# Kernel tuning notes

Hardware: AMD Instinct MI355X
Metric: run time of the kernel (lower is better)

## Reference

```python
import jax, jax.numpy as jnp
import numpy as np

N = 50000      # nodes
E = 400000     # lower-adjacency edges (avg degree 8)
D = 128        # input_dim == output_dim (o_dim in DEC_HOGNN)
GEO = 20       # geo_dim
H = 3          # heads
C = 128        # out_channels per head
NUM_LAYERS = 3


def _lin_init(key, fan_in, fan_out, extra=()):
    s = 1.0 / np.sqrt(fan_in)
    return jax.random.uniform(key, extra + (fan_in, fan_out), jnp.float32, -s, s)


def setup_inputs() -> dict:
    key = jax.random.key(0)
    ks = jax.random.split(key, 20)
    inp = {
        "h": jax.random.normal(ks[0], (N, D), jnp.float32),
        "lower_adj_feat": jax.random.normal(ks[1], (E, GEO), jnp.float32),
        "dir_w": jax.random.normal(ks[2], (E, 1), jnp.float32),
        "src_idx": jax.random.randint(ks[3], (E,), 0, N),
        "dst_idx": jax.random.randint(ks[4], (E,), 0, N),
        # edge_encoder: Linear(2*D + geo + 1 -> D)
        "W_ee": _lin_init(ks[5], 2 * D + GEO + 1, D),
        "b_ee": jnp.zeros((D,), jnp.float32),
        # residual linear (layer 0 only; others Identity)
        "W_res": _lin_init(ks[6], D, D),
        "b_res": jnp.zeros((D,), jnp.float32),
        # 3 TransformerConv layers, all in=D out=C heads=H (stacked)
        "Wq": _lin_init(ks[7], D, H * C, (NUM_LAYERS,)),
        "bq": jnp.zeros((NUM_LAYERS, H * C), jnp.float32),
        "Wk": _lin_init(ks[8], D, H * C, (NUM_LAYERS,)),
        "bk": jnp.zeros((NUM_LAYERS, H * C), jnp.float32),
        "Wv": _lin_init(ks[9], D, H * C, (NUM_LAYERS,)),
        "bv": jnp.zeros((NUM_LAYERS, H * C), jnp.float32),
        "We": _lin_init(ks[10], D, H * C, (NUM_LAYERS,)),
        "be": jnp.zeros((NUM_LAYERS, H * C), jnp.float32),
        # lin_skip: in -> out_channels (concat=False)
        "Ws": _lin_init(ks[11], D, C, (NUM_LAYERS,)),
        "bs": jnp.zeros((NUM_LAYERS, C), jnp.float32),
        # ctr_lin: Linear(input_dim + output_dim -> output_dim)
        "W_ctr": _lin_init(ks[12], 2 * D, D),
        "b_ctr": jnp.zeros((D,), jnp.float32),
    }
    return inp


def _transformer_conv(x, src, dst, e_attr, Wq, bq, Wk, bk, Wv, bv, We, be, Ws, bs):
    """PyG TransformerConv, heads=H, concat=False (head mean), root skip."""
    n = x.shape[0]
    q = (x @ Wq + bq).reshape(n, H, C)
    k = (x @ Wk + bk).reshape(n, H, C)
    v = (x @ Wv + bv).reshape(n, H, C)
    e = (e_attr @ We + be).reshape(-1, H, C)      # [E,H,C]
    ke = k[src] + e                                # edge-conditioned keys
    alpha = (q[dst] * ke).sum(-1) / jnp.sqrt(jnp.asarray(C, x.dtype))  # [E,H]
    # segment softmax over destination nodes
    amax = jax.ops.segment_max(alpha, dst, num_segments=n)
    amax = jnp.where(jnp.isfinite(amax), amax, 0.0)
    ex = jnp.exp(alpha - amax[dst])
    den = jax.ops.segment_sum(ex, dst, num_segments=n)
    w = ex / (den[dst] + 1e-16)
    msg = (v[src] + e) * w[:, :, None]             # [E,H,C]
    out = jax.ops.segment_sum(msg.reshape(-1, H * C), dst, num_segments=n)
    out = out.reshape(n, H, C).mean(axis=1)        # concat=False -> head mean
    return out + x @ Ws + bs                       # root weight skip


def reference(h, lower_adj_feat, dir_w, src_idx, dst_idx,
              W_ee, b_ee, W_res, b_res,
              Wq, bq, Wk, bk, Wv, bv, We, be, Ws, bs,
              W_ctr, b_ctr):
    # edge encoder: [h[dst], h[src]*dir, dir, geo] -> D
    edge_features = jnp.concatenate(
        [h[dst_idx], h[src_idx] * dir_w, dir_w, lower_adj_feat], axis=-1)
    edge_attr = edge_features @ W_ee + b_ee
    h_cur = h
    for i in range(NUM_LAYERS):
        residual = (h_cur @ W_res + b_res) if i == 0 else h_cur
        h_t = _transformer_conv(h_cur, src_idx, dst_idx, edge_attr,
                                Wq[i], bq[i], Wk[i], bk[i], Wv[i], bv[i],
                                We[i], be[i], Ws[i], bs[i])
        h_cur = jax.nn.relu(h_t + residual)
    return jnp.concatenate([h, h_cur], axis=-1) @ W_ctr + b_ctr
```

## Files before the change

### kernel.cpp

```cpp
#include <hip/hip_runtime.h>
#include <math.h>

#define NN 50000
#define NE 400000

typedef _Float16 f16;
typedef _Float16 f16x8 __attribute__((ext_vector_type(8)));
typedef _Float16 f16x4 __attribute__((ext_vector_type(4)));
typedef _Float16 f16x2 __attribute__((ext_vector_type(2)));
typedef float f32x4 __attribute__((ext_vector_type(4)));

static __device__ __forceinline__ float dot8(f16x8 a, f16x8 b, float acc) {
#if defined(__has_builtin) && __has_builtin(__builtin_amdgcn_fdot2)
#pragma unroll
  for (int j = 0; j < 4; ++j) {
    f16x2 x = {a[2 * j], a[2 * j + 1]};
    f16x2 y = {b[2 * j], b[2 * j + 1]};
    acc = __builtin_amdgcn_fdot2(x, y, acc, false);
  }
#else
#pragma unroll
  for (int j = 0; j < 8; ++j) acc += (float)a[j] * (float)b[j];
#endif
  return acc;
}

#if defined(__has_builtin) && __has_builtin(__builtin_amdgcn_global_load_lds)
#define HAVE_GLL 1
static __device__ __forceinline__ void gload_lds16(const f16* gp, f16* lp) {
  __builtin_amdgcn_global_load_lds((const __attribute__((address_space(1))) void*)gp,
                                   (__attribute__((address_space(3))) void*)lp, 16, 0, 0);
}
#else
#define HAVE_GLL 0
#endif

__global__ __launch_bounds__(256) void hgemm_k128_kernel(
    const f16* __restrict__ A, int lda,
    const f16* __restrict__ WT,
    const float* __restrict__ bias,
    f16* __restrict__ outb, int ldb,
    int M, int ntiles)
{
  __shared__ f16 As[128 * 128];
  __shared__ f16 Bs[64 * 128];
  const int t = threadIdx.x;
  const int wv = t >> 6, lane = t & 63;
  const int l15 = lane & 15, l4 = lane >> 4;
  const int c8 = lane & 15, rsub = lane >> 4;
  const int row0 = blockIdx.x * 128;

#if HAVE_GLL
#pragma unroll
  for (int k = 0; k < 8; ++k) {
    int r = wv * 4 + k * 16 + rsub;
    int rc = row0 + r; if (rc >= M) rc = M - 1;
    const f16* gp = A + (size_t)rc * lda + ((c8 ^ (r & 15)) << 3);
    gload_lds16(gp, As + (wv * 4 + k * 16) * 128);
  }
#else
  for (int i = t; i < 2048; i += 256) {
    int r = i >> 4, cc = i & 15;
    int gr = row0 + r; if (gr >= M) gr = M - 1;
    float4 v = *(const float4*)(A + (size_t)gr * lda + cc * 8);
    *(float4*)(As + r * 128 + ((cc ^ (r & 15)) << 3)) = v;
  }
#endif
  for (int ct = 0; ct < ntiles; ++ct) {
    const int col0 = (blockIdx.y * ntiles + ct) * 64;
#if HAVE_GLL
#pragma unroll
    for (int k = 0; k < 4; ++k) {
      int c = wv * 4 + k * 16 + rsub;
      const f16* gp = WT + (size_t)(col0 + c) * 128 + ((c8 ^ (c & 15)) << 3);
      gload_lds16(gp, Bs + (wv * 4 + k * 16) * 128);
    }
#else
    for (int i = t; i < 1024; i += 256) {
      int c = i >> 4, cc = i & 15;
      float4 v = *(const float4*)(WT + (size_t)(col0 + c) * 128 + cc * 8);
      *(float4*)(Bs + c * 128 + ((cc ^ (c & 15)) << 3)) = v;
    }
#endif
    __syncthreads();
    f32x4 acc[2][4];
#pragma unroll
    for (int m = 0; m < 2; ++m)
#pragma unroll
      for (int n = 0; n < 4; ++n) acc[m][n] = (f32x4){0.f, 0.f, 0.f, 0.f};
#pragma unroll
    for (int ks = 0; ks < 4; ++ks) {
      const int co = (((ks * 4 + l4) ^ l15) << 3);
      f16x8 a0 = *(const f16x8*)(As + (wv * 32 +      l15) * 128 + co);
      f16x8 a1 = *(const f16x8*)(As + (wv * 32 + 16 + l15) * 128 + co);
      f16x8 b0 = *(const f16x8*)(Bs + (     l15) * 128 + co);
      f16x8 b1 = *(const f16x8*)(Bs + (16 + l15) * 128 + co);
      f16x8 b2 = *(const f16x8*)(Bs + (32 + l15) * 128 + co);
      f16x8 b3 = *(const f16x8*)(Bs + (48 + l15) * 128 + co);
      acc[0][0] = __builtin_amdgcn_mfma_f32_16x16x32_f16(a0, b0, acc[0][0], 0, 0, 0);
      acc[0][1] = __builtin_amdgcn_mfma_f32_16x16x32_f16(a0, b1, acc[0][1], 0, 0, 0);
      acc[0][2] = __builtin_amdgcn_mfma_f32_16x16x32_f16(a0, b2, acc[0][2], 0, 0, 0);
      acc[0][3] = __builtin_amdgcn_mfma_f32_16x16x32_f16(a0, b3, acc[0][3], 0, 0, 0);
      acc[1][0] = __builtin_amdgcn_mfma_f32_16x16x32_f16(a1, b0, acc[1][0], 0, 0, 0);
      acc[1][1] = __builtin_amdgcn_mfma_f32_16x16x32_f16(a1, b1, acc[1][1], 0, 0, 0);
      acc[1][2] = __builtin_amdgcn_mfma_f32_16x16x32_f16(a1, b2, acc[1][2], 0, 0, 0);
      acc[1][3] = __builtin_amdgcn_mfma_f32_16x16x32_f16(a1, b3, acc[1][3], 0, 0, 0);
    }
    __syncthreads();
    float bv4[4];
#pragma unroll
    for (int n = 0; n < 4; ++n) bv4[n] = bias ? bias[col0 + n * 16 + l15] : 0.f;
#pragma unroll
    for (int m = 0; m < 2; ++m) {
#pragma unroll
      for (int j = 0; j < 4; ++j) {
        int r = row0 + wv * 32 + m * 16 + l4 * 4 + j;
        if (r >= M) continue;
#pragma unroll
        for (int n = 0; n < 4; ++n) {
          int c = col0 + n * 16 + l15;
          outb[(size_t)r * ldb + c] = (f16)(acc[m][n][j] + bv4[n]);
        }
      }
    }
  }
}

__global__ __launch_bounds__(256) void hgemm2_kernel(
    const f16* __restrict__ A, int lda,
    const f16* __restrict__ A2, int lda2, int a2k,
    const f16* __restrict__ WT, int K,
    const float* __restrict__ bias,
    float* __restrict__ outf,
    f16* __restrict__ outb, int ldb,
    const f16* __restrict__ fresid, int ldr,
    int dorelu, int M)
{
  __shared__ f16 As[128 * 128];
  __shared__ f16 Bs[128 * 128];
  const int t = threadIdx.x;
  const int wv = t >> 6, lane = t & 63;
  const int l15 = lane & 15, l4 = lane >> 4;
  const int c8 = lane & 15, rsub = lane >> 4;
  const int row0 = blockIdx.x * 128;
  const int col0 = blockIdx.y * 128;

  f32x4 acc[2][8];
#pragma unroll
  for (int m = 0; m < 2; ++m)
#pragma unroll
    for (int n = 0; n < 8; ++n) acc[m][n] = (f32x4){0.f, 0.f, 0.f, 0.f};

  for (int kc = 0; kc < K; kc += 128) {
    const f16* Ap; int koff, ldA;
    if (kc >= a2k) { Ap = A2; koff = kc - a2k; ldA = lda2; }
    else           { Ap = A;  koff = kc;       ldA = lda;  }
#if HAVE_GLL
#pragma unroll
    for (int k = 0; k < 8; ++k) {
      int r = wv * 4 + k * 16 + rsub;
      int rc = row0 + r; if (rc >= M) rc = M - 1;
      const f16* gp = Ap + (size_t)rc * ldA + koff + ((c8 ^ (r & 15)) << 3);
      gload_lds16(gp, As + (wv * 4 + k * 16) * 128);
    }
#pragma unroll
    for (int k = 0; k < 8; ++k) {
      int c = wv * 4 + k * 16 + rsub;
      const f16* gp = WT + (size_t)(col0 + c) * K + kc + ((c8 ^ (c & 15)) << 3);
      gload_lds16(gp, Bs + (wv * 4 + k * 16) * 128);
    }
#else
    for (int i = t; i < 2048; i += 256) {
      int r = i >> 4, cc = i & 15;
      int gr = row0 + r; if (gr >= M) gr = M - 1;
      float4 v = *(const float4*)(Ap + (size_t)gr * ldA + koff + cc * 8);
      *(float4*)(As + r * 128 + ((cc ^ (r & 15)) << 3)) = v;
    }
    for (int i = t; i < 2048; i += 256) {
      int c = i >> 4, cc = i & 15;
      float4 v = *(const float4*)(WT + (size_t)(col0 + c) * K + kc + cc * 8);
      *(float4*)(Bs + c * 128 + ((cc ^ (c & 15)) << 3)) = v;
    }
#endif
    __syncthreads();
#pragma unroll
    for (int ks = 0; ks < 4; ++ks) {
      const int co = (((ks * 4 + l4) ^ l15) << 3);
      f16x8 a0 = *(const f16x8*)(As + (wv * 32 +      l15) * 128 + co);
      f16x8 a1 = *(const f16x8*)(As + (wv * 32 + 16 + l15) * 128 + co);
#pragma unroll
      for (int n = 0; n < 8; ++n) {
        f16x8 b = *(const f16x8*)(Bs + (n * 16 + l15) * 128 + co);
        acc[0][n] = __builtin_amdgcn_mfma_f32_16x16x32_f16(a0, b, acc[0][n], 0, 0, 0);
        acc[1][n] = __builtin_amdgcn_mfma_f32_16x16x32_f16(a1, b, acc[1][n], 0, 0, 0);
      }
    }
    __syncthreads();
  }

  float bv8[8];
#pragma unroll
  for (int n = 0; n < 8; ++n) bv8[n] = bias ? bias[col0 + n * 16 + l15] : 0.f;
#pragma unroll
  for (int m = 0; m < 2; ++m) {
#pragma unroll
    for (int j = 0; j < 4; ++j) {
      int r = row0 + wv * 32 + m * 16 + l4 * 4 + j;
      if (r >= M) continue;
#pragma unroll
      for (int n = 0; n < 8; ++n) {
        int c = col0 + n * 16 + l15;
        float val = acc[m][n][j] + bv8[n];
        if (fresid) val += (float)fresid[(size_t)r * ldr + c];
        if (dorelu) val = fmaxf(val, 0.f);
        if (outb) outb[(size_t)r * ldb + c] = (f16)val;
        else      outf[(size_t)r * 128 + c] = val;
      }
    }
  }
}

__global__ void zero_int_kernel(int* __restrict__ p, int n) {
  int i = blockIdx.x * 256 + threadIdx.x;
  if (i < n) p[i] = 0;
}
__global__ void hist_kernel(const int* __restrict__ dst, int* __restrict__ deg) {
  int e = blockIdx.x * 256 + threadIdx.x;
  if (e < NE) atomicAdd(&deg[dst[e]], 1);
}
__global__ void scanA_kernel(const int* __restrict__ deg, int* __restrict__ rowstart,
                             int* __restrict__ part) {
  __shared__ int sd[256];
  int b = blockIdx.x, t = threadIdx.x, i = b * 256 + t;
  sd[t] = (i < NN) ? deg[i] : 0;
  __syncthreads();
  for (int o = 1; o < 256; o <<= 1) {
    int v = (t >= o) ? sd[t - o] : 0;
    __syncthreads();
    sd[t] += v;
    __syncthreads();
  }
  if (i < NN) rowstart[i + 1] = sd[t];
  if (t == 255) part[b] = sd[255];
}
__global__ void scanB_kernel(int* __restrict__ part, int nb) {
  __shared__ int sd[256];
  int t = threadIdx.x;
  sd[t] = (t < nb) ? part[t] : 0;
  __syncthreads();
  for (int o = 1; o < 256; o <<= 1) {
    int v = (t >= o) ? sd[t - o] : 0;
    __syncthreads();
    sd[t] += v;
    __syncthreads();
  }
  if (t < nb) part[t] = sd[t];
}
__global__ void scanC_kernel(const int* __restrict__ deg, int* __restrict__ rowstart,
                             const int* __restrict__ part, int* __restrict__ cursor) {
  int b = blockIdx.x, t = threadIdx.x, i = b * 256 + t;
  if (i >= NN) return;
  int off = b ? part[b - 1] : 0;
  int fin = rowstart[i + 1] + off;
  rowstart[i + 1] = fin;
  cursor[i] = fin - deg[i];
  if (i == 0) rowstart[0] = 0;
}
__global__ void scatter_kernel(const int* __restrict__ dst, const int* __restrict__ src,
                               const float* __restrict__ dirw, const float* __restrict__ geo,
                               int* __restrict__ cursor,
                               int* __restrict__ srcp, f16* __restrict__ dirpb,
                               f16* __restrict__ geop) {
  int e = blockIdx.x * 256 + threadIdx.x;
  if (e < NE) {
    int pos = atomicAdd(&cursor[dst[e]], 1);
    srcp[pos] = src[e];
    float dv = dirw[e];
    dirpb[pos] = (f16)dv;
    f16* gp = geop + (size_t)pos * 24;
#pragma unroll
    for (int j = 0; j < 20; ++j) gp[j] = (f16)geo[(size_t)e * 20 + j];
    gp[20] = (f16)dv;
    gp[21] = (f16)0.f; gp[22] = (f16)0.f; gp[23] = (f16)0.f;
  }
}

__global__ void prep_kernel(const float* __restrict__ Wee, const float* __restrict__ bee,
                            const float* __restrict__ WeAll, const float* __restrict__ beAll,
                            float* __restrict__ matsAll)
{
  const int layer = blockIdx.y;
  const float* We = WeAll + (size_t)layer * 49152;
  const float* be = beAll + (size_t)layer * 384;
  float* mats = matsAll + (size_t)layer * 132352;
  int idx = blockIdx.x * 256 + threadIdx.x;
  if (idx >= 132352) return;
  float acc = 0.0f;
  if (idx < 49152) {
    int h = idx >> 14, rem = idx & 16383, c = rem >> 7, u = rem & 127;
    for (int j = 0; j < 128; ++j)
      acc += We[(size_t)j * 384 + h * 128 + c] * Wee[(size_t)(128 + u) * 128 + j];
    mats[idx] = acc;
  } else if (idx < 58368) {
    int r = idx - 49152; int h = r / 3072; int rem = r - h * 3072; int c = rem / 24; int u = rem - c * 24;
    if (u < 21) {
      int trow = (u < 20) ? (257 + u) : 256;
      for (int j = 0; j < 128; ++j)
        acc += We[(size_t)j * 384 + h * 128 + c] * Wee[(size_t)trow * 128 + j];
    }
    mats[idx] = acc;
  } else if (idx < 107520) {
    int r = idx - 58368; int h = r >> 14; int rem = r & 16383; int tt = rem >> 7; int c = rem & 127;
    for (int j = 0; j < 128; ++j)
      acc += Wee[(size_t)(128 + tt) * 128 + j] * We[(size_t)j * 384 + h * 128 + c];
    mats[idx] = acc;
  } else if (idx < 115584) {
    int r = idx - 107520; int h = r / 2688; int rem = r - h * 2688; int tt = rem >> 7; int c = rem & 127;
    int trow = (tt < 20) ? (257 + tt) : 256;
    for (int j = 0; j < 128; ++j)
      acc += Wee[(size_t)trow * 128 + j] * We[(size_t)j * 384 + h * 128 + c];
    mats[idx] = acc;
  } else if (idx < 115968) {
    int r = idx - 115584; int h = r >> 7; int c = r & 127;
    for (int j = 0; j < 128; ++j)
      acc += bee[j] * We[(size_t)j * 384 + h * 128 + c];
    mats[idx] = acc + be[h * 128 + c];
  } else {
    int r = idx - 115968; int tt = r >> 7; int c = r & 127;
    for (int j = 0; j < 128; ++j)
      acc += Wee[(size_t)tt * 128 + j] *
             (We[(size_t)j * 384 + c] + We[(size_t)j * 384 + 128 + c] + We[(size_t)j * 384 + 256 + c]);
    mats[idx] = acc * (1.0f / 3.0f);
  }
}

__global__ void prepB_kernel(const float* __restrict__ Wq, const float* __restrict__ bq,
                             const float* __restrict__ Wk, const float* __restrict__ matsAll,
                             f16* __restrict__ WABT, float* __restrict__ biasAB)
{
  int idx = blockIdx.x * 256 + threadIdx.x;
  if (idx < 344064) {
    int i = idx / 114688; int r = idx % 114688; int c = r >> 7; int k = r & 127;
    float acc = 0.f;
    if (c < 384) {
      int h = c >> 7, u = c & 127;
      const float* wq = Wq + ((size_t)i * 128 + k) * 384 + h * 128;
      const float* wk = Wk + ((size_t)i * 128 + u) * 384 + h * 128;
      for (int c2 = 0; c2 < 128; ++c2) acc += wq[c2] * wk[c2];
    } else if (c < 768) {
      int h = (c - 384) >> 7, u = (c - 384) & 127;
      const float* wq = Wq + ((size_t)i * 128 + k) * 384 + h * 128;
      const float* m2 = matsAll + (size_t)i * 132352 + h * 16384 + u;
      for (int c2 = 0; c2 < 128; ++c2) acc += wq[c2] * m2[c2 * 128];
    } else if (c < 840) {
      int h = (c - 768) / 24, tt = (c - 768) % 24;
      const float* wq = Wq + ((size_t)i * 128 + k) * 384 + h * 128;
      const float* m34 = matsAll + (size_t)i * 132352 + 49152 + h * 3072 + tt;
      for (int c2 = 0; c2 < 128; ++c2) acc += wq[c2] * m34[c2 * 24];
    }
    WABT[(size_t)i * 114688 + c * 128 + k] = (f16)acc;
  } else if (idx < 346752) {
    int r = idx - 344064; int i = r / 896; int c = r % 896;
    float acc = 0.f;
    if (c < 384) {
      int h = c >> 7, u = c & 127;
      const float* bqv = bq + i * 384 + h * 128;
      const float* wk = Wk + ((size_t)i * 128 + u) * 384 + h * 128;
      for (int c2 = 0; c2 < 128; ++c2) acc += bqv[c2] * wk[c2];
    } else if (c < 768) {
      int h = (c - 384) >> 7, u = (c - 384) & 127;
      const float* bqv = bq + i * 384 + h * 128;
      const float* m2 = matsAll + (size_t)i * 132352 + h * 16384 + u;
      for (int c2 = 0; c2 < 128; ++c2) acc += bqv[c2] * m2[c2 * 128];
    } else if (c < 840) {
      int h = (c - 768) / 24, tt = (c - 768) % 24;
      const float* bqv = bq + i * 384 + h * 128;
      const float* m34 = matsAll + (size_t)i * 132352 + 49152 + h * 3072 + tt;
      for (int c2 = 0; c2 < 128; ++c2) acc += bqv[c2] * m34[c2 * 24];
    }
    biasAB[i * 896 + c] = acc;
  }
}

__global__ void prep2_kernel(const float* __restrict__ matsAll, const float* __restrict__ Wv,
                             const float* __restrict__ bv, const float* __restrict__ Ws,
                             const float* __restrict__ Wres, f16* __restrict__ W2bigT)
{
  int idx = blockIdx.x * 256 + threadIdx.x;
  if (idx >= 442368) return;
  int i = idx / 147456; int r = idx % 147456; int c = r / 1152; int k = r % 1152;
  float v = 0.f;
  if (k < 384) {
    int h = k >> 7, tt = k & 127;
    v = matsAll[(size_t)i * 132352 + 58368 + h * 16384 + tt * 128 + c];
  } else if (k < 768) {
    int h = (k - 384) >> 7, u = (k - 384) & 127;
    v = Wv[((size_t)i * 128 + u) * 384 + h * 128 + c];
  } else if (k < 840) {
    int h = (k - 768) / 24, tt = (k - 768) % 24;
    if (tt < 21)       v = matsAll[(size_t)i * 132352 + 107520 + h * 2688 + tt * 128 + c];
    else if (tt == 21) v = matsAll[(size_t)i * 132352 + 115584 + h * 128 + c]
                         + bv[i * 384 + h * 128 + c];
  } else if (k < 896) {
    v = 0.f;
  } else if (k < 1024) {
    v = matsAll[(size_t)i * 132352 + 115968 + (k - 896) * 128 + c];
  } else {
    v = Ws[((size_t)i * 128 + (k - 1024)) * 128 + c];
    if (i == 0) v += Wres[(k - 1024) * 128 + c];
  }
  W2bigT[(size_t)i * 147456 + c * 1152 + k] = (f16)v;
}

__global__ void wprep_kernel(const float* __restrict__ Wctr, const float* __restrict__ bs,
                             const float* __restrict__ bres,
                             f16* __restrict__ WctrT2, float* __restrict__ bias0)
{
  int idx = blockIdx.x * 256 + threadIdx.x;
  if (idx < 32768) {
    int c = idx >> 8, k = idx & 255;
    float v = (k < 128) ? Wctr[(size_t)(128 + k) * 128 + c]
                        : Wctr[(size_t)(k - 128) * 128 + c];
    WctrT2[idx] = (f16)v;
  } else if (idx < 32896) {
    int c = idx - 32768;
    bias0[c] = bs[c] + bres[c];
  }
}

__global__ __launch_bounds__(256) void attn_kernel(
    const f16* __restrict__ xh,
    f16* __restrict__ nbuf,
    const int* __restrict__ rowstart,
    const int* __restrict__ srcp,
    const f16* __restrict__ dirpb,
    const f16* __restrict__ geop)
{
  const int sl = threadIdx.x & 15;
  const int n = blockIdx.x * 16 + (threadIdx.x >> 4);
  const float rsC = 0.088388347648318447f;
  f16* row = nbuf + (size_t)n * 1024;

  f16x8 qk[3], g2[3];
#pragma unroll
  for (int h = 0; h < 3; ++h) {
    qk[h] = *(const f16x8*)(row + h * 128 + sl * 8);
    g2[h] = *(const f16x8*)(row + 384 + h * 128 + sl * 8);
  }
  float g34a[3], g34c[3];
#pragma unroll
  for (int h = 0; h < 3; ++h) {
    g34a[h] = (float)row[768 + h * 24 + sl];
    g34c[h] = (sl < 8) ? (float)row[768 + h * 24 + 16 + sl] : 0.f;
  }
  float den[3] = {0.f, 0.f, 0.f};
  float F2[3][8], Fv[3][8];
#pragma unroll
  for (int h = 0; h < 3; ++h)
#pragma unroll
    for (int j = 0; j < 8; ++j) { F2[h][j] = 0.f; Fv[h][j] = 0.f; }
  float f34a[3] = {0.f, 0.f, 0.f}, f34c[3] = {0.f, 0.f, 0.f};

  const int beg = rowstart[n], end = rowstart[n + 1];
  int ii = beg;
  for (; ii + 1 < end; ii += 2) {
    const int s0 = srcp[ii], s1 = srcp[ii + 1];
    const float d0 = (float)dirpb[ii], d1 = (float)dirpb[ii + 1];
    const f16* p0 = xh + (size_t)s0 * 256 + sl * 8;
    const f16* p1 = xh + (size_t)s1 * 256 + sl * 8;
    f16x8 xv0 = *(const f16x8*)p0;
    f16x8 hv0 = *(const f16x8*)(p0 + 128);
    f16x8 xv1 = *(const f16x8*)p1;
    f16x8 hv1 = *(const f16x8*)(p1 + 128);
    const float gea0 = (float)geop[(size_t)ii * 24 + sl];
    const float geb0 = (sl < 8) ? (float)geop[(size_t)ii * 24 + 16 + sl] : 0.f;
    const float gea1 = (float)geop[(size_t)(ii + 1) * 24 + sl];
    const float geb1 = (sl < 8) ? (float)geop[(size_t)(ii + 1) * 24 + 16 + sl] : 0.f;

    float pa[6];
#pragma unroll
    for (int h = 0; h < 3; ++h) {
      pa[h]     = dot8(qk[h], xv0, 0.f) + d0 * dot8(g2[h], hv0, 0.f)
                + gea0 * g34a[h] + geb0 * g34c[h];
      pa[3 + h] = dot8(qk[h], xv1, 0.f) + d1 * dot8(g2[h], hv1, 0.f)
                + gea1 * g34a[h] + geb1 * g34c[h];
    }
#pragma unroll
    for (int off = 1; off < 16; off <<= 1) {
#pragma unroll
      for (int q = 0; q < 6; ++q) pa[q] += __shfl_xor(pa[q], off);
    }
    float w0[3], w1[3];
#pragma unroll
    for (int h = 0; h < 3; ++h) {
      w0[h] = __expf(pa[h] * rsC);
      w1[h] = __expf(pa[3 + h] * rsC);
      den[h] += w0[h] + w1[h];
    }
#pragma unroll
    for (int h = 0; h < 3; ++h) {
      const float wd0 = w0[h] * d0, wd1 = w1[h] * d1;
#pragma unroll
      for (int j = 0; j < 8; ++j) {
        F2[h][j] = fmaf(wd0, (float)hv0[j], fmaf(wd1, (float)hv1[j], F2[h][j]));
        Fv[h][j] = fmaf(w0[h], (float)xv0[j], fmaf(w1[h], (float)xv1[j], Fv[h][j]));
      }
      f34a[h] = fmaf(w0[h], gea0, fmaf(w1[h], gea1, f34a[h]));
      f34c[h] = fmaf(w0[h], geb0, fmaf(w1[h], geb1, f34c[h]));
    }
  }
  if (ii < end) {
    const int s0 = srcp[ii];
    const float d0 = (float)dirpb[ii];
    const f16* p0 = xh + (size_t)s0 * 256 + sl * 8;
    f16x8 xv0 = *(const f16x8*)p0;
    f16x8 hv0 = *(const f16x8*)(p0 + 128);
    const float gea0 = (float)geop[(size_t)ii * 24 + sl];
    const float geb0 = (sl < 8) ? (float)geop[(size_t)ii * 24 + 16 + sl] : 0.f;
    float pa[3];
#pragma unroll
    for (int h = 0; h < 3; ++h)
      pa[h] = dot8(qk[h], xv0, 0.f) + d0 * dot8(g2[h], hv0, 0.f)
            + gea0 * g34a[h] + geb0 * g34c[h];
#pragma unroll
    for (int off = 1; off < 16; off <<= 1) {
#pragma unroll
      for (int q = 0; q < 3; ++q) pa[q] += __shfl_xor(pa[q], off);
    }
#pragma unroll
    for (int h = 0; h < 3; ++h) {
      const float w = __expf(pa[h] * rsC);
      den[h] += w;
      const float wd = w * d0;
#pragma unroll
      for (int j = 0; j < 8; ++j) {
        F2[h][j] = fmaf(wd, (float)hv0[j], F2[h][j]);
        Fv[h][j] = fmaf(w, (float)xv0[j], Fv[h][j]);
      }
      f34a[h] = fmaf(w, gea0, f34a[h]);
      f34c[h] = fmaf(w, geb0, f34c[h]);
    }
  }

  float sc[3], swh[3];
#pragma unroll
  for (int h = 0; h < 3; ++h) {
    sc[h] = (1.f / 3.f) / (den[h] + 1e-16f);
    swh[h] = den[h] * sc[h];
  }
#pragma unroll
  for (int h = 0; h < 3; ++h) {
    f16x8 o1, o2;
#pragma unroll
    for (int j = 0; j < 8; ++j) {
      o1[j] = (f16)(F2[h][j] * sc[h]);
      o2[j] = (f16)(Fv[h][j] * sc[h]);
    }
    *(f16x8*)(row + h * 128 + sl * 8) = o1;
    *(f16x8*)(row + 384 + h * 128 + sl * 8) = o2;
  }
#pragma unroll
  for (int h = 0; h < 3; ++h) {
    row[768 + h * 24 + sl] = (f16)(f34a[h] * sc[h]);
    if (sl < 8) {
      float fcv = (sl == 5) ? swh[h] : f34c[h] * sc[h];
      row[768 + h * 24 + 16 + sl] = (f16)fcv;
    }
  }
  f16x8 ho = *(const f16x8*)(xh + (size_t)n * 256 + 128 + sl * 8);
  if (beg >= end) {
#pragma unroll
    for (int j = 0; j < 8; ++j) ho[j] = (f16)0.f;
  }
  *(f16x8*)(row + 896 + sl * 8) = ho;
}

__global__ void hconv_kernel(const float* __restrict__ src, f16* __restrict__ xh) {
  int i = blockIdx.x * 256 + threadIdx.x;
  if (i >= NN * 32) return;
  float4 a = ((const float4*)src)[i];
  f16x4 o;
  o[0] = (f16)a.x; o[1] = (f16)a.y; o[2] = (f16)a.z; o[3] = (f16)a.w;
  int r = i >> 5, c4 = i & 31;
  *(f16x4*)(xh + (size_t)r * 256 + c4 * 4) = o;
  *(f16x4*)(xh + (size_t)r * 256 + 128 + c4 * 4) = o;
}

extern "C" void kernel_launch(void* const* d_in, const int* in_sizes, int n_in,
                              void* d_out, int out_size, void* d_ws, size_t ws_size,
                              hipStream_t stream)
{
  (void)in_sizes; (void)n_in; (void)out_size; (void)ws_size;
  const float* h    = (const float*)d_in[0];
  const float* geo  = (const float*)d_in[1];
  const float* dirw = (const float*)d_in[2];
  const int*   src  = (const int*)d_in[3];
  const int*   dst  = (const int*)d_in[4];
  const float* Wee  = (const float*)d_in[5];
  const float* bee  = (const float*)d_in[6];
  const float* Wres = (const float*)d_in[7];
  const float* bres = (const float*)d_in[8];
  const float* Wq   = (const float*)d_in[9];
  const float* bq   = (const float*)d_in[10];
  const float* Wk   = (const float*)d_in[11];
  const float* bk   = (const float*)d_in[12];  (void)bk;
  const float* Wv   = (const float*)d_in[13];
  const float* bv   = (const float*)d_in[14];
  const float* We   = (const float*)d_in[15];
  const float* be   = (const float*)d_in[16];
  const float* Ws   = (const float*)d_in[17];
  const float* bs   = (const float*)d_in[18];
  const float* Wctr = (const float*)d_in[19];
  const float* bctr = (const float*)d_in[20];

  char* base = (char*)d_ws;
  size_t off = 0;
  auto take = [&](size_t bytes) -> char* {
    char* p = base + off;
    off += bytes;
    off = (off + 255) & ~(size_t)255;
    return p;
  };
  f16* nbuf     = (f16*)take((size_t)NN * 1024 * 2);
  f16* xh       = (f16*)take((size_t)NN * 256 * 2);
  float* mats   = (float*)take((size_t)3 * 132352 * 4);
  f16* WABT     = (f16*)take((size_t)3 * 114688 * 2);
  float* biasAB = (float*)take((size_t)3 * 896 * 4);
  f16* W2bigT   = (f16*)take((size_t)3 * 147456 * 2);
  f16* WctrT2   = (f16*)take(32768 * 2);
  float* bias0  = (float*)take(128 * 4);
  f16* dirpb    = (f16*)take((size_t)NE * 2);
  f16* geop     = (f16*)take((size_t)NE * 24 * 2);
  int* deg      = (int*)take((size_t)NN * 4);
  int* rowstart = (int*)take((size_t)(NN + 1) * 4);
  int* cursor   = (int*)take((size_t)NN * 4);
  int* srcp     = (int*)take((size_t)NE * 4);
  int* part     = (int*)take(256 * 4);

  zero_int_kernel<<<(NN + 255) / 256, 256, 0, stream>>>(deg, NN);
  hist_kernel<<<(NE + 255) / 256, 256, 0, stream>>>(dst, deg);
  scanA_kernel<<<196, 256, 0, stream>>>(deg, rowstart, part);
  scanB_kernel<<<1, 256, 0, stream>>>(part, 196);
  scanC_kernel<<<196, 256, 0, stream>>>(deg, rowstart, part, cursor);
  scatter_kernel<<<(NE + 255) / 256, 256, 0, stream>>>(dst, src, dirw, geo, cursor,
                                                       srcp, dirpb, geop);
  hconv_kernel<<<6250, 256, 0, stream>>>(h, xh);
  wprep_kernel<<<129, 256, 0, stream>>>(Wctr, bs, bres, WctrT2, bias0);
  prep_kernel<<<dim3(518, 3), 256, 0, stream>>>(Wee, bee, We, be, mats);
  prepB_kernel<<<(346752 + 255) / 256, 256, 0, stream>>>(Wq, bq, Wk, mats, WABT, biasAB);
  prep2_kernel<<<(442368 + 255) / 256, 256, 0, stream>>>(mats, Wv, bv, Ws, Wres, W2bigT);

  for (int i = 0; i < 3; ++i) {
    hgemm_k128_kernel<<<dim3(391, 2), 256, 0, stream>>>(xh, 256, WABT + (size_t)i * 114688,
        biasAB + (size_t)i * 896, nbuf, 1024, NN, 7);
    attn_kernel<<<3125, 256, 0, stream>>>(xh, nbuf, rowstart, srcp, dirpb, geop);
    const float* obias = (i == 0) ? bias0 : (bs + i * 128);
    const f16* resid = (i == 0) ? nullptr : xh;
    hgemm2_kernel<<<dim3(391, 1), 256, 0, stream>>>(nbuf, 1024, xh, 256, 1024,
        W2bigT + (size_t)i * 147456, 1152, obias, nullptr, xh, 256,
        resid, 256, 1, NN);
  }
  hgemm2_kernel<<<dim3(391, 1), 256, 0, stream>>>(xh, 256, nullptr, 256, 1 << 30,
      WctrT2, 256, bctr, (float*)d_out, nullptr, 0, nullptr, 0, 0, NN);
}
```

Before: 609.5 us.

## Fuse final ctr_lin GEMM into last layer's output GEMM epilogue

In the last layer, the output GEMM kernel now writes its relu'd fp16 tile into shared memory and immediately multiplies it by the ctr_lin weights. It then loads the original h half from xh and accumulates it, writing the final fp32 output directly. This removes a separate kernel launch and a re-read of the hidden state from global memory. In exchange it adds extra shared-memory traffic and synchronisation to that block, and clamps out-of-range rows when loading.

```diff
diff --git a/kernel.cpp b/kernel.cpp
--- a/kernel.cpp
+++ b/kernel.cpp
@@ -131,10 +131,11 @@
     const f16* __restrict__ A2, int lda2, int a2k,
     const f16* __restrict__ WT, int K,
     const float* __restrict__ bias,
-    float* __restrict__ outf,
     f16* __restrict__ outb, int ldb,
     const f16* __restrict__ fresid, int ldr,
-    int dorelu, int M)
+    int dorelu, int M,
+    const f16* __restrict__ ctrW, const float* __restrict__ ctrB,
+    float* __restrict__ ctrOut)
 {
   __shared__ f16 As[128 * 128];
   __shared__ f16 Bs[128 * 128];
@@ -205,16 +206,82 @@
   for (int m = 0; m < 2; ++m) {
 #pragma unroll
     for (int j = 0; j < 4; ++j) {
-      int r = row0 + wv * 32 + m * 16 + l4 * 4 + j;
-      if (r >= M) continue;
+      int rl = wv * 32 + m * 16 + l4 * 4 + j;
+      int r = row0 + rl;
 #pragma unroll
       for (int n = 0; n < 8; ++n) {
         int c = col0 + n * 16 + l15;
         float val = acc[m][n][j] + bv8[n];
         if (fresid) val += (float)fresid[(size_t)r * ldr + c];
         if (dorelu) val = fmaxf(val, 0.f);
-        if (outb) outb[(size_t)r * ldb + c] = (f16)val;
-        else      outf[(size_t)r * 128 + c] = val;
+        f16 hv = (f16)val;
+        if (r < M) outb[(size_t)r * ldb + c] = hv;
+        if (ctrOut)
+          As[rl * 128 + (((c >> 3) ^ (rl & 15)) << 3) + (c & 7)] = hv;
+      }
+    }
+  }
+
+  if (ctrOut) {
+    for (int i = t; i < 2048; i += 256) {
+      int c = i >> 4, k8 = i & 15;
+      float4 v = *(const float4*)(ctrW + (size_t)c * 256 + k8 * 8);
+      *(float4*)(Bs + c * 128 + ((k8 ^ (c & 15)) << 3)) = v;
+    }
+    __syncthreads();
+    f32x4 acc2[2][8];
+#pragma unroll
+    for (int m = 0; m < 2; ++m)
+#pragma unroll
+      for (int n = 0; n < 8; ++n) acc2[m][n] = (f32x4){0.f, 0.f, 0.f, 0.f};
+#pragma unroll
+    for (int ks = 0; ks < 4; ++ks) {
+      const int co = (((ks * 4 + l4) ^ l15) << 3);
+      f16x8 a0 = *(const f16x8*)(As + (wv * 32 +      l15) * 128 + co);
+      f16x8 a1 = *(const f16x8*)(As + (wv * 32 + 16 + l15) * 128 + co);
+#pragma unroll
+      for (int n = 0; n < 8; ++n) {
+        f16x8 b = *(const f16x8*)(Bs + (n * 16 + l15) * 128 + co);
+        acc2[0][n] = __builtin_amdgcn_mfma_f32_16x16x32_f16(a0, b, acc2[0][n], 0, 0, 0);
+        acc2[1][n] = __builtin_amdgcn_mfma_f32_16x16x32_f16(a1, b, acc2[1][n], 0, 0, 0);
+      }
+    }
+    __syncthreads();
+    for (int i = t; i < 2048; i += 256) {
+      int r = i >> 4, k8 = i & 15;
+      int gr = row0 + r; if (gr >= M) gr = M - 1;
+      float4 v = *(const float4*)(A2 + (size_t)gr * lda2 + 128 + k8 * 8);
+      *(float4*)(As + r * 128 + ((k8 ^ (r & 15)) << 3)) = v;
+    }
+    for (int i = t; i < 2048; i += 256) {
+      int c = i >> 4, k8 = i & 15;
+      float4 v = *(const float4*)(ctrW + (size_t)c * 256 + 128 + k8 * 8);
+      *(float4*)(Bs + c * 128 + ((k8 ^ (c & 15)) << 3)) = v;
+    }
+    __syncthreads();
+#pragma unroll
+    for (int ks = 0; ks < 4; ++ks) {
+      const int co = (((ks * 4 + l4) ^ l15) << 3);
+      f16x8 a0 = *(const f16x8*)(As + (wv * 32 +      l15) * 128 + co);
+      f16x8 a1 = *(const f16x8*)(As + (wv * 32 + 16 + l15) * 128 + co);
+#pragma unroll
+      for (int n = 0; n < 8; ++n) {
+        f16x8 b = *(const f16x8*)(Bs + (n * 16 + l15) * 128 + co);
+        acc2[0][n] = __builtin_amdgcn_mfma_f32_16x16x32_f16(a0, b, acc2[0][n], 0, 0, 0);
+        acc2[1][n] = __builtin_amdgcn_mfma_f32_16x16x32_f16(a1, b, acc2[1][n], 0, 0, 0);
+      }
+    }
+#pragma unroll
+    for (int m = 0; m < 2; ++m) {
+#pragma unroll
+      for (int j = 0; j < 4; ++j) {
+        int r = row0 + wv * 32 + m * 16 + l4 * 4 + j;
+        if (r >= M) continue;
+#pragma unroll
+        for (int n = 0; n < 8; ++n) {
+          int c = n * 16 + l15;
+          ctrOut[(size_t)r * 128 + c] = acc2[m][n][j] + ctrB[c];
+        }
       }
     }
   }
@@ -656,10 +723,11 @@
     attn_kernel<<<3125, 256, 0, stream>>>(xh, nbuf, rowstart, srcp, dirpb, geop);
     const float* obias = (i == 0) ? bias0 : (bs + i * 128);
     const f16* resid = (i == 0) ? nullptr : xh;
+    const f16* ctrW = (i == 2) ? WctrT2 : nullptr;
+    const float* ctrB = (i == 2) ? bctr : nullptr;
+    float* ctrOut = (i == 2) ? (float*)d_out : nullptr;
     hgemm2_kernel<<<dim3(391, 1), 256, 0, stream>>>(nbuf, 1024, xh, 256, 1024,
-        W2bigT + (size_t)i * 147456, 1152, obias, nullptr, xh, 256,
-        resid, 256, 1, NN);
-  }
-  hgemm2_kernel<<<dim3(391, 1), 256, 0, stream>>>(xh, 256, nullptr, 256, 1 << 30,
-      WctrT2, 256, bctr, (float*)d_out, nullptr, 0, nullptr, 0, 0, NN);
-}
+        W2bigT + (size_t)i * 147456, 1152, obias, xh, 256,
+        resid, 256, 1, NN, ctrW, ctrB, ctrOut);
+  }
+}
```

After: 602.5 us. About the same (-1.1%).
